# Performance work log

Measured on AMD Instinct MI355X. Metric: run time of the kernel, lower is better.

Reference implementation:

```python
import jax, jax.numpy as jnp
import numpy as np

EPS = 1e-3
GRIDSIZE = 100
MAX_ITER = 3


def _project(x, kf):
    """Euclidean projection onto {y in [0,1]^dim : sum(y) = k} via grid bisection.

    x: [bs, dim] float; kf: [bs] float (number of selected entries per row).
    Returns y = clip(x + nu, 0, 1).
    """
    bs, dim = x.shape
    ki = jnp.round(kf).astype(jnp.int32)                       # [bs]
    xsorted = -jnp.sort(-x, axis=-1)                           # descending sort, [bs, dim]
    nulow = -jnp.take_along_axis(xsorted, (ki - 1)[:, None], axis=-1)[:, 0]  # [bs]
    nuup = nulow + 1.0
    grid01 = jnp.linspace(0.0, 1.0, GRIDSIZE, dtype=x.dtype)   # [G]

    def search_row(res_row, k_val):
        return jnp.searchsorted(res_row, k_val)                # side='left' matches torch

    for _ in range(MAX_ITER):
        delta = nuup - nulow                                   # [bs]
        active = delta > EPS                                   # rows still refining
        nugrid = nulow[:, None] + grid01[None, :] * delta[:, None]        # [bs, G]
        # res[b, g] = sum_j clip(x[b, j] + nugrid[b, g], 0, 1)  -- monotone increasing in g
        res = jnp.clip(x[:, None, :] + nugrid[:, :, None], 0.0, 1.0).sum(-1)  # [bs, G]
        upix = jax.vmap(search_row)(res, kf)                   # [bs]
        upix = jnp.clip(upix, 1, GRIDSIZE - 1)
        new_up = jnp.take_along_axis(nugrid, upix[:, None], axis=-1)[:, 0]
        new_low = jnp.take_along_axis(nugrid, (upix - 1)[:, None], axis=-1)[:, 0]
        nuup = jnp.where(active, new_up, nuup)
        nulow = jnp.where(active, new_low, nulow)

    nu = 0.5 * (nulow + nuup)                                  # [bs]
    y = jnp.clip(x + nu[:, None], 0.0, 1.0)                    # [bs, dim]
    return y


def setup_inputs() -> dict:
    key = jax.random.key(0)
    bs, dim, k0 = 512, 4096, 512
    x = jax.random.normal(key, (bs, dim), dtype=jnp.float32)
    k = jnp.full((bs,), k0, dtype=jnp.int32)                   # forward uses k[0] for topk
    return {"x": x, "k": k, "k0": k0}


def reference(x, k, k0):
    kf = k.astype(x.dtype)
    soft = _project(x, kf)                                     # [bs, dim]
    # hard top-k mask using k0 = k[0] (static), scattered into zeros
    _, sel = jax.lax.top_k(soft, k0)                           # [bs, k0]
    rows = jnp.arange(soft.shape[0])[:, None]
    hard = jnp.zeros_like(soft).at[rows, sel].set(1.0)
    # straight-through estimator: forward = hard, backward = soft's grad
    return jax.lax.stop_gradient(hard - soft) + soft
```

## Files before the change

### kernel.cpp

```cpp
#include <hip/hip_runtime.h>


#define DIM  4096
#define EPL  8
#define NC0  16
#define CPAD 260

__device__ __forceinline__ void select_bin(const int4 h, const int lane, const int kr,
                                           int& chosen, int& cumG, int& T) {
    const int s3 = h.w, s2 = h.z + s3, s1 = h.y + s2, s0 = h.x + s1;
    int v = s0;
    #pragma unroll
    for (int off = 1; off < 64; off <<= 1) {
        int t = __shfl_down(v, off, 64);
        if (lane + off < 64) v += t;
    }
    const int inc = v - s0;
    const int S0 = s0 + inc, S1 = s1 + inc, S2 = s2 + inc, S3 = s3 + inc;
    int ci, cg, Tl;
    if      (S3 >= kr) { ci = 3; cg = inc; Tl = h.w; }
    else if (S2 >= kr) { ci = 2; cg = S3;  Tl = h.z; }
    else if (S1 >= kr) { ci = 1; cg = S2;  Tl = h.y; }
    else               { ci = 0; cg = S1;  Tl = h.x; }
    const bool has = (S0 >= kr) && (inc < kr);
    const unsigned long long m = __ballot(has);
    const int src = __ffsll((unsigned long long)m) - 1;
    chosen = __shfl((lane << 2) + ci, src, 64);
    cumG   = __shfl(cg, src, 64);
    T      = __shfl(Tl, src, 64);
}

__global__ void __launch_bounds__(512)
topk_mask_kernel(const float* __restrict__ x, const int* __restrict__ k0ptr,
                 float* __restrict__ out) {
    const int tid  = threadIdx.x;
    const int lane = tid & 63;
    const int w    = tid >> 6;
    const int row  = blockIdx.x;

    const float4* xr4   = (const float4*)(x   + (size_t)row * DIM);
    float4*       outr4 = (float4*)      (out + (size_t)row * DIM);

    __shared__ int hist0[NC0 * CPAD];
    __shared__ int histp[3][256];
    __shared__ unsigned int surv[64];
    __shared__ int scnt;
    __shared__ int wtie[8];

    const int k0 = k0ptr[0];

    const float4 f0 = xr4[(w << 7) + lane];
    const float4 f1 = xr4[(w << 7) + 64 + lane];

    for (int t = tid; t < NC0 * CPAD; t += 512) hist0[t] = 0;
    for (int t = tid; t < 3 * 256;   t += 512) ((int*)histp)[t] = 0;
    if (tid == 0) scnt = 0;

    unsigned int u[EPL];
#define MAP4(i, vv)                                                        \
    {                                                                      \
        unsigned int b0 = __float_as_uint((vv).x);                         \
        unsigned int b1 = __float_as_uint((vv).y);                         \
        unsigned int b2 = __float_as_uint((vv).z);                         \
        unsigned int b3 = __float_as_uint((vv).w);                         \
        u[4*(i)+0] = (b0 & 0x80000000u) ? ~b0 : (b0 | 0x80000000u);        \
        u[4*(i)+1] = (b1 & 0x80000000u) ? ~b1 : (b1 | 0x80000000u);        \
        u[4*(i)+2] = (b2 & 0x80000000u) ? ~b2 : (b2 | 0x80000000u);        \
        u[4*(i)+3] = (b3 & 0x80000000u) ? ~b3 : (b3 | 0x80000000u);        \
    }
    MAP4(0, f0) MAP4(1, f1)
#undef MAP4

    __syncthreads();

    const int c0 = ((((w & 1) << 3) | (lane & 7))) * CPAD;
    #pragma unroll
    for (int j = 0; j < EPL; ++j)
        atomicAdd(&hist0[c0 + (u[j] >> 24)], 1);
    __syncthreads();

    int kr = k0;
    int4 h; h.x = 0; h.y = 0; h.z = 0; h.w = 0;
    #pragma unroll
    for (int c = 0; c < NC0; ++c) {
        const int4 t = *(const int4*)&hist0[c * CPAD + (lane << 2)];
        h.x += t.x; h.y += t.y; h.z += t.z; h.w += t.w;
    }
    int chosen, cumG, T;
    select_bin(h, lane, kr, chosen, cumG, T);
    kr -= cumG;
    unsigned int pfx = ((unsigned int)chosen) << 24;

    #pragma unroll
    for (int j = 0; j < EPL; ++j)
        if ((u[j] >> 24) == (pfx >> 24))
            atomicAdd(&histp[0][(u[j] >> 16) & 255u], 1);
    __syncthreads();
    h = *(const int4*)&histp[0][lane << 2];
    select_bin(h, lane, kr, chosen, cumG, T);
    kr -= cumG;
    pfx |= ((unsigned int)chosen) << 16;

    unsigned int thr;
    if (T <= 64) {
        #pragma unroll
        for (int j = 0; j < EPL; ++j)
            if ((u[j] & 0xFFFF0000u) == pfx) {
                const int slot = atomicAdd(&scnt, 1);
                surv[slot] = u[j];
            }
        __syncthreads();
        const unsigned int v = (lane < T) ? surv[lane] : 0u;
        bool act = (lane < T);
        #pragma unroll
        for (int b = 15; b >= 0; --b) {
            const unsigned int bit = (v >> b) & 1u;
            const unsigned long long m1 = __ballot(act && (bit != 0u));
            const int c = __popcll(m1);
            const bool ge = (c >= kr);
            act = act && (bit == (ge ? 1u : 0u));
            if (!ge) kr -= c;
        }
        const unsigned long long ma = __ballot(act);
        T   = __popcll(ma);
        thr = __shfl(v, __ffsll((unsigned long long)ma) - 1, 64);
    } else {
        #pragma unroll
        for (int j = 0; j < EPL; ++j)
            if ((u[j] & 0xFFFF0000u) == pfx)
                atomicAdd(&histp[1][(u[j] >> 8) & 255u], 1);
        __syncthreads();
        h = *(const int4*)&histp[1][lane << 2];
        select_bin(h, lane, kr, chosen, cumG, T);
        kr -= cumG;
        pfx |= ((unsigned int)chosen) << 8;

        #pragma unroll
        for (int j = 0; j < EPL; ++j)
            if ((u[j] & 0xFFFFFF00u) == pfx)
                atomicAdd(&histp[2][u[j] & 255u], 1);
        __syncthreads();
        h = *(const int4*)&histp[2][lane << 2];
        select_bin(h, lane, kr, chosen, cumG, T);
        kr -= cumG;
        thr = pfx | (unsigned int)chosen;
    }

    if (kr == T) {
        #pragma unroll
        for (int i = 0; i < 2; ++i) {
            float4 o;
            o.x = (u[4*i+0] >= thr) ? 1.0f : 0.0f;
            o.y = (u[4*i+1] >= thr) ? 1.0f : 0.0f;
            o.z = (u[4*i+2] >= thr) ? 1.0f : 0.0f;
            o.w = (u[4*i+3] >= thr) ? 1.0f : 0.0f;
            outr4[(w << 7) + (i << 6) + lane] = o;
        }
    } else {
        int eqtot = 0;
        #pragma unroll
        for (int j = 0; j < EPL; ++j) eqtot += (u[j] == thr) ? 1 : 0;
        int vv = eqtot;
        #pragma unroll
        for (int off = 1; off < 64; off <<= 1) {
            int t = __shfl_up(vv, off, 64);
            if (lane >= off) vv += t;
        }
        if (lane == 63) wtie[w] = vv;
        __syncthreads();
        int base = 0;
        #pragma unroll
        for (int ww = 0; ww < 8; ++ww) if (ww < w) base += wtie[ww];

        #pragma unroll
        for (int i = 0; i < 2; ++i) {
            const int e0 = (u[4*i+0] == thr) ? 1 : 0;
            const int e1 = (u[4*i+1] == thr) ? 1 : 0;
            const int e2 = (u[4*i+2] == thr) ? 1 : 0;
            const int e3 = (u[4*i+3] == thr) ? 1 : 0;
            const int ti = e0 + e1 + e2 + e3;
            int vi = ti;
            #pragma unroll
            for (int off = 1; off < 64; off <<= 1) {
                int t = __shfl_up(vi, off, 64);
                if (lane >= off) vi += t;
            }
            int r = base + (vi - ti);
            const int tot = __shfl(vi, 63, 64);
            float4 o;
            o.x = (u[4*i+0] > thr) ? 1.0f : ((e0 && r < kr) ? 1.0f : 0.0f); r += e0;
            o.y = (u[4*i+1] > thr) ? 1.0f : ((e1 && r < kr) ? 1.0f : 0.0f); r += e1;
            o.z = (u[4*i+2] > thr) ? 1.0f : ((e2 && r < kr) ? 1.0f : 0.0f); r += e2;
            o.w = (u[4*i+3] > thr) ? 1.0f : ((e3 && r < kr) ? 1.0f : 0.0f); r += e3;
            outr4[(w << 7) + (i << 6) + lane] = o;
            base += tot;
        }
    }
}

extern "C" void kernel_launch(void* const* d_in, const int* in_sizes, int n_in,
                              void* d_out, int out_size, void* d_ws, size_t ws_size,
                              hipStream_t stream) {
    const float* x   = (const float*)d_in[0];
    const int*   k0  = (const int*)d_in[2];
    float*       out = (float*)d_out;

    const int bs = in_sizes[1];
    topk_mask_kernel<<<bs, 512, 0, stream>>>(x, k0, out);
}
```

Before: 11.95 us.

## Process two rows per block with upfront loads and nontemporal stores

Each 512-thread block now handles two rows. Both rows' inputs are loaded and mapped to sortable keys up front, and the rows are then processed one after the other through a templated per-row radix-select, so the second row's global load latency is hidden. Per-row histogram buffers are duplicated in shared memory, and the first-level histogram copies are now indexed by warp and lane parity instead of lane&7. Output stores use nontemporal builtins. The grid shrinks to 256 blocks, which is about one block per CU on a 256-CU part, but the second row's selection is serialized and shared-memory use roughly doubles.

```diff
diff --git a/kernel.cpp b/kernel.cpp
--- a/kernel.cpp
+++ b/kernel.cpp
@@ -5,6 +5,22 @@
 #define EPL  8
 #define NC0  16
 #define CPAD 260
+
+typedef float nfloat4 __attribute__((ext_vector_type(4)));
+
+__device__ __forceinline__ void nt_store4(float4* p, const float4 o) {
+    nfloat4 n; n.x = o.x; n.y = o.y; n.z = o.z; n.w = o.w;
+    __builtin_nontemporal_store(n, (nfloat4*)p);
+}
+
+struct Shared {
+    int hist0[2][NC0 * CPAD];
+    int hist1[2][256];
+    int histf[2][256];
+    unsigned int surv[2][64];
+    int scnt[2];
+    int wtie[8];
+};
 
 __device__ __forceinline__ void select_bin(const int4 h, const int lane, const int kr,
                                            int& chosen, int& cumG, int& T) {
@@ -30,91 +46,60 @@
     T      = __shfl(Tl, src, 64);
 }
 
-__global__ void __launch_bounds__(512)
-topk_mask_kernel(const float* __restrict__ x, const int* __restrict__ k0ptr,
-                 float* __restrict__ out) {
-    const int tid  = threadIdx.x;
-    const int lane = tid & 63;
-    const int w    = tid >> 6;
-    const int row  = blockIdx.x;
-
-    const float4* xr4   = (const float4*)(x   + (size_t)row * DIM);
-    float4*       outr4 = (float4*)      (out + (size_t)row * DIM);
-
-    __shared__ int hist0[NC0 * CPAD];
-    __shared__ int histp[3][256];
-    __shared__ unsigned int surv[64];
-    __shared__ int scnt;
-    __shared__ int wtie[8];
-
-    const int k0 = k0ptr[0];
-
-    const float4 f0 = xr4[(w << 7) + lane];
-    const float4 f1 = xr4[(w << 7) + 64 + lane];
-
-    for (int t = tid; t < NC0 * CPAD; t += 512) hist0[t] = 0;
-    for (int t = tid; t < 3 * 256;   t += 512) ((int*)histp)[t] = 0;
-    if (tid == 0) scnt = 0;
-
-    unsigned int u[EPL];
-#define MAP4(i, vv)                                                        \
-    {                                                                      \
-        unsigned int b0 = __float_as_uint((vv).x);                         \
-        unsigned int b1 = __float_as_uint((vv).y);                         \
-        unsigned int b2 = __float_as_uint((vv).z);                         \
-        unsigned int b3 = __float_as_uint((vv).w);                         \
-        u[4*(i)+0] = (b0 & 0x80000000u) ? ~b0 : (b0 | 0x80000000u);        \
-        u[4*(i)+1] = (b1 & 0x80000000u) ? ~b1 : (b1 | 0x80000000u);        \
-        u[4*(i)+2] = (b2 & 0x80000000u) ? ~b2 : (b2 | 0x80000000u);        \
-        u[4*(i)+3] = (b3 & 0x80000000u) ? ~b3 : (b3 | 0x80000000u);        \
-    }
-    MAP4(0, f0) MAP4(1, f1)
-#undef MAP4
-
-    __syncthreads();
-
-    const int c0 = ((((w & 1) << 3) | (lane & 7))) * CPAD;
+template <int R>
+__device__ __forceinline__ void process_row(const unsigned int (&u)[EPL], Shared& sm,
+                                            float4* __restrict__ outr4,
+                                            const int k0, const int lane, const int w) {
+    const int c0 = ((w << 1) | (lane & 1)) * CPAD;
     #pragma unroll
     for (int j = 0; j < EPL; ++j)
-        atomicAdd(&hist0[c0 + (u[j] >> 24)], 1);
+        atomicAdd(&sm.hist0[R][c0 + (u[j] >> 24)], 1);
     __syncthreads();
 
     int kr = k0;
-    int4 h; h.x = 0; h.y = 0; h.z = 0; h.w = 0;
-    #pragma unroll
-    for (int c = 0; c < NC0; ++c) {
-        const int4 t = *(const int4*)&hist0[c * CPAD + (lane << 2)];
-        h.x += t.x; h.y += t.y; h.z += t.z; h.w += t.w;
-    }
-    int chosen, cumG, T;
-    select_bin(h, lane, kr, chosen, cumG, T);
-    kr -= cumG;
-    unsigned int pfx = ((unsigned int)chosen) << 24;
+    unsigned int pfx;
+    int T;
+    {
+        int4 h; h.x = 0; h.y = 0; h.z = 0; h.w = 0;
+        #pragma unroll
+        for (int c = 0; c < NC0; ++c) {
+            const int4 t = *(const int4*)&sm.hist0[R][c * CPAD + (lane << 2)];
+            h.x += t.x; h.y += t.y; h.z += t.z; h.w += t.w;
+        }
+        int ch, cg, Tx;
+        select_bin(h, lane, kr, ch, cg, Tx);
+        kr -= cg;
+        pfx = ((unsigned int)ch) << 24;
+    }
 
     #pragma unroll
     for (int j = 0; j < EPL; ++j)
-        if ((u[j] >> 24) == (pfx >> 24))
-            atomicAdd(&histp[0][(u[j] >> 16) & 255u], 1);
+        if ((u[j] & 0xFF000000u) == pfx)
+            atomicAdd(&sm.hist1[R][(u[j] >> 16) & 255u], 1);
     __syncthreads();
-    h = *(const int4*)&histp[0][lane << 2];
-    select_bin(h, lane, kr, chosen, cumG, T);
-    kr -= cumG;
-    pfx |= ((unsigned int)chosen) << 16;
+    {
+        const int4 h = *(const int4*)&sm.hist1[R][lane << 2];
+        int ch, cg, Tx;
+        select_bin(h, lane, kr, ch, cg, Tx);
+        kr -= cg;
+        pfx |= ((unsigned int)ch) << 16;
+        T = Tx;
+    }
 
     unsigned int thr;
     if (T <= 64) {
         #pragma unroll
         for (int j = 0; j < EPL; ++j)
             if ((u[j] & 0xFFFF0000u) == pfx) {
-                const int slot = atomicAdd(&scnt, 1);
-                surv[slot] = u[j];
+                const int slot = atomicAdd(&sm.scnt[R], 1);
+                sm.surv[R][slot] = u[j];
             }
         __syncthreads();
-        const unsigned int v = (lane < T) ? surv[lane] : 0u;
+        const unsigned int vv = (lane < T) ? sm.surv[R][lane] : 0u;
         bool act = (lane < T);
         #pragma unroll
         for (int b = 15; b >= 0; --b) {
-            const unsigned int bit = (v >> b) & 1u;
+            const unsigned int bit = (vv >> b) & 1u;
             const unsigned long long m1 = __ballot(act && (bit != 0u));
             const int c = __popcll(m1);
             const bool ge = (c >= kr);
@@ -123,27 +108,36 @@
         }
         const unsigned long long ma = __ballot(act);
         T   = __popcll(ma);
-        thr = __shfl(v, __ffsll((unsigned long long)ma) - 1, 64);
+        thr = __shfl(vv, __ffsll((unsigned long long)ma) - 1, 64);
     } else {
         #pragma unroll
         for (int j = 0; j < EPL; ++j)
             if ((u[j] & 0xFFFF0000u) == pfx)
-                atomicAdd(&histp[1][(u[j] >> 8) & 255u], 1);
-        __syncthreads();
-        h = *(const int4*)&histp[1][lane << 2];
-        select_bin(h, lane, kr, chosen, cumG, T);
-        kr -= cumG;
-        pfx |= ((unsigned int)chosen) << 8;
-
+                atomicAdd(&sm.histf[0][(u[j] >> 8) & 255u], 1);
+        __syncthreads();
+        {
+            const int4 h = *(const int4*)&sm.histf[0][lane << 2];
+            int ch, cg, Tx;
+            select_bin(h, lane, kr, ch, cg, Tx);
+            kr -= cg;
+            pfx |= ((unsigned int)ch) << 8;
+        }
         #pragma unroll
         for (int j = 0; j < EPL; ++j)
             if ((u[j] & 0xFFFFFF00u) == pfx)
-                atomicAdd(&histp[2][u[j] & 255u], 1);
-        __syncthreads();
-        h = *(const int4*)&histp[2][lane << 2];
-        select_bin(h, lane, kr, chosen, cumG, T);
-        kr -= cumG;
-        thr = pfx | (unsigned int)chosen;
+                atomicAdd(&sm.histf[1][u[j] & 255u], 1);
+        __syncthreads();
+        {
+            const int4 h = *(const int4*)&sm.histf[1][lane << 2];
+            int ch, cg, Tx;
+            select_bin(h, lane, kr, ch, cg, Tx);
+            kr -= cg;
+            thr = pfx | (unsigned int)ch;
+            T = Tx;
+        }
+        __syncthreads();
+        ((int*)sm.histf)[(w << 6) | lane] = 0;
+        __syncthreads();
     }
 
     if (kr == T) {
@@ -154,7 +148,7 @@
             o.y = (u[4*i+1] >= thr) ? 1.0f : 0.0f;
             o.z = (u[4*i+2] >= thr) ? 1.0f : 0.0f;
             o.w = (u[4*i+3] >= thr) ? 1.0f : 0.0f;
-            outr4[(w << 7) + (i << 6) + lane] = o;
+            nt_store4(&outr4[(w << 7) + (i << 6) + lane], o);
         }
     } else {
         int eqtot = 0;
@@ -166,11 +160,11 @@
             int t = __shfl_up(vv, off, 64);
             if (lane >= off) vv += t;
         }
-        if (lane == 63) wtie[w] = vv;
+        if (lane == 63) sm.wtie[w] = vv;
         __syncthreads();
         int base = 0;
         #pragma unroll
-        for (int ww = 0; ww < 8; ++ww) if (ww < w) base += wtie[ww];
+        for (int ww = 0; ww < 8; ++ww) if (ww < w) base += sm.wtie[ww];
 
         #pragma unroll
         for (int i = 0; i < 2; ++i) {
@@ -192,10 +186,62 @@
             o.y = (u[4*i+1] > thr) ? 1.0f : ((e1 && r < kr) ? 1.0f : 0.0f); r += e1;
             o.z = (u[4*i+2] > thr) ? 1.0f : ((e2 && r < kr) ? 1.0f : 0.0f); r += e2;
             o.w = (u[4*i+3] > thr) ? 1.0f : ((e3 && r < kr) ? 1.0f : 0.0f); r += e3;
-            outr4[(w << 7) + (i << 6) + lane] = o;
+            nt_store4(&outr4[(w << 7) + (i << 6) + lane], o);
             base += tot;
         }
     }
+}
+
+__global__ void __launch_bounds__(512)
+topk_mask_kernel(const float* __restrict__ x, const int* __restrict__ k0ptr,
+                 float* __restrict__ out, const int bs) {
+    const int tid  = threadIdx.x;
+    const int lane = tid & 63;
+    const int w    = tid >> 6;
+    const int row0 = (int)(blockIdx.x << 1);
+    const int row1 = row0 + 1;
+    const bool has1 = (row1 < bs);
+
+    __shared__ Shared sm;
+
+    const float4* xr0 = (const float4*)(x + (size_t)row0 * DIM);
+    const float4* xr1 = (const float4*)(x + (size_t)(has1 ? row1 : row0) * DIM);
+    float4* or0 = (float4*)(out + (size_t)row0 * DIM);
+    float4* or1 = (float4*)(out + (size_t)row1 * DIM);
+
+    const int k0 = k0ptr[0];
+
+    const int base = (w << 7) + lane;
+    const float4 f0 = xr0[base];
+    const float4 f1 = xr0[base + 64];
+    const float4 g0 = xr1[base];
+    const float4 g1 = xr1[base + 64];
+
+    for (int t = tid; t < 2 * NC0 * CPAD; t += 512) ((int*)sm.hist0)[t] = 0;
+    ((int*)sm.hist1)[tid] = 0;
+    ((int*)sm.histf)[tid] = 0;
+    if (tid < 2) sm.scnt[tid] = 0;
+
+    unsigned int u[EPL], v[EPL];
+#define MAP4(arr, i, vv)                                                    \
+    {                                                                       \
+        unsigned int b0 = __float_as_uint((vv).x);                          \
+        unsigned int b1 = __float_as_uint((vv).y);                          \
+        unsigned int b2 = __float_as_uint((vv).z);                          \
+        unsigned int b3 = __float_as_uint((vv).w);                          \
+        arr[4*(i)+0] = (b0 & 0x80000000u) ? ~b0 : (b0 | 0x80000000u);       \
+        arr[4*(i)+1] = (b1 & 0x80000000u) ? ~b1 : (b1 | 0x80000000u);       \
+        arr[4*(i)+2] = (b2 & 0x80000000u) ? ~b2 : (b2 | 0x80000000u);       \
+        arr[4*(i)+3] = (b3 & 0x80000000u) ? ~b3 : (b3 | 0x80000000u);       \
+    }
+    MAP4(u, 0, f0) MAP4(u, 1, f1)
+    MAP4(v, 0, g0) MAP4(v, 1, g1)
+#undef MAP4
+
+    __syncthreads();
+
+    process_row<0>(u, sm, or0, k0, lane, w);
+    if (has1) process_row<1>(v, sm, or1, k0, lane, w);
 }
 
 extern "C" void kernel_launch(void* const* d_in, const int* in_sizes, int n_in,
@@ -206,5 +252,6 @@
     float*       out = (float*)d_out;
 
     const int bs = in_sizes[1];
-    topk_mask_kernel<<<bs, 512, 0, stream>>>(x, k0, out);
-}
+    const int grid = (bs + 1) >> 1;
+    topk_mask_kernel<<<grid, 512, 0, stream>>>(x, k0, out, bs);
+}
```

New measurement: 17.91 us. 1.5x slower.
